# Kernel tuning notes

Hardware: AMD Instinct MI355X
Metric: run time of the kernel (lower is better)

## Reference

```python
import jax, jax.numpy as jnp
import numpy as np

N = 100000   # nodes
E = 1600000  # edges (avg degree 16)
F = 64       # in_feats
H = 128      # hidden_size
O = 10       # out_feats
L = 3        # SAGEConv layers
EPS = 1e-5


def setup_inputs() -> dict:
    key = jax.random.key(0)
    ks = jax.random.split(key, 16)
    s = 0.05
    return {
        "nodes": jax.random.normal(ks[0], (N, F), jnp.float32),
        "src": jax.random.randint(ks[1], (E,), 0, N),
        "dst": jax.random.randint(ks[2], (E,), 0, N),
        # input MLP: Linear(F,H) -> ReLU -> Linear(H,H)
        "W_in1": jax.random.normal(ks[3], (F, H), jnp.float32) * s,
        "b_in1": jnp.zeros((H,), jnp.float32),
        "W_in2": jax.random.normal(ks[4], (H, H), jnp.float32) * s,
        "b_in2": jnp.zeros((H,), jnp.float32),
        # L stacked SAGEConv layers (mean aggregator)
        "W_self": jax.random.normal(ks[5], (L, H, H), jnp.float32) * s,
        "W_neigh": jax.random.normal(ks[6], (L, H, H), jnp.float32) * s,
        "b_sage": jnp.zeros((L, H), jnp.float32),
        "ln_g": jnp.ones((L, H), jnp.float32),
        "ln_b": jnp.zeros((L, H), jnp.float32),
        # output head Linear(H, O)
        "W_out": jax.random.normal(ks[7], (H, O), jnp.float32) * s,
        "b_out": jnp.zeros((O,), jnp.float32),
    }


def reference(nodes, src, dst, W_in1, b_in1, W_in2, b_in2,
              W_self, W_neigh, b_sage, ln_g, ln_b, W_out, b_out):
    # input MLP
    h = jax.nn.relu(nodes @ W_in1 + b_in1) @ W_in2 + b_in2  # [N, H]

    # in-degree for mean aggregation (0-degree nodes get 0 neighbor feature)
    deg = jax.ops.segment_sum(jnp.ones((E,), h.dtype), dst, num_segments=N)
    inv_deg = (1.0 / jnp.maximum(deg, 1.0))[:, None]  # [N, 1]

    for l in range(L):
        # mean over incoming neighbors: gather src feats, scatter-add to dst
        agg = jax.ops.segment_sum(h[src], dst, num_segments=N) * inv_deg  # [N, H]
        h = h @ W_self[l] + agg @ W_neigh[l] + b_sage[l]
        h = jax.nn.relu(h)
        # LayerNorm over feature dim
        mu = h.mean(-1, keepdims=True)
        var = h.var(-1, keepdims=True)
        h = ln_g[l] * (h - mu) * jax.lax.rsqrt(var + EPS) + ln_b[l]

    # dgl.mean_nodes over the single graph -> [1, H]
    g = h.mean(0, keepdims=True)
    return g @ W_out + b_out  # [1, O]
```

## Files before the change

kernel.cpp:

```cpp
#include <hip/hip_runtime.h>
#include <hip/hip_bf16.h>

#define NN 100000
#define NE 1600000
#define FF 64
#define HH 128
#define OO 10
#define NL 3
#define NB 391
#define NBLK 1000
#define CHUNK 1600
#define BCAP 5376
#define LNEPS 1e-5f

typedef short s8v __attribute__((ext_vector_type(8)));
typedef float f32x4 __attribute__((ext_vector_type(4)));
typedef float f32x2 __attribute__((ext_vector_type(2)));

__device__ __forceinline__ unsigned short f2b(float f){
  unsigned u = __float_as_uint(f);
  unsigned r = (u + 0x7FFFu + ((u>>16)&1u)) >> 16;
  return (unsigned short)r;
}

#if __has_builtin(__builtin_amdgcn_cvt_pk_f32_fp8) && __has_builtin(__builtin_amdgcn_cvt_pk_fp8_f32)
__device__ __forceinline__ unsigned char f8enc(float x){
  int p = __builtin_amdgcn_cvt_pk_fp8_f32(x, x, 0, false);
  return (unsigned char)(p & 0xFF);
}
__device__ __forceinline__ void f8dec4(unsigned u, float* o){
  f32x2 lo = __builtin_amdgcn_cvt_pk_f32_fp8(u, false);
  f32x2 hi = __builtin_amdgcn_cvt_pk_f32_fp8(u, true);
  o[0]=lo[0]; o[1]=lo[1]; o[2]=hi[0]; o[3]=hi[1];
}
#else
#include <hip/hip_fp8.h>
__device__ __forceinline__ unsigned char f8enc(float x){
  __hip_fp8_e4m3 q(x); return (unsigned char)q.__x;
}
__device__ __forceinline__ void f8dec4(unsigned u, float* o){
  for(int i=0;i<4;i++){
    __hip_fp8_e4m3 q; q.__x = (unsigned char)(u>>(8*i));
    o[i] = (float)q;
  }
}
#endif

__global__ __launch_bounds__(256) void k_bcount(const int* __restrict__ dst, int* __restrict__ bcnt,
                                                int* __restrict__ blockcnt){
  __shared__ int h[NB];
  for(int i=threadIdx.x;i<NB;i+=256) h[i]=0;
  __syncthreads();
  int base = blockIdx.x*CHUNK;
  for(int i=threadIdx.x;i<CHUNK;i+=256){
    int e = base+i;
    if(e<NE) atomicAdd(&h[((unsigned)dst[e])>>8],1);
  }
  __syncthreads();
  for(int i=threadIdx.x;i<NB;i+=256){
    int v=h[i];
    blockcnt[i*1024 + blockIdx.x] = v;
    if(v) atomicAdd(&bcnt[i],v);
  }
}

__global__ void k_bscan(const int* __restrict__ bcnt, int* __restrict__ boff, int* __restrict__ rowoff){
  __shared__ int s[512];
  int t=threadIdx.x;
  int v = (t<NB)? bcnt[t]:0;
  s[t]=v; __syncthreads();
  for(int off=1;off<512;off<<=1){
    int x=(t>=off)?s[t-off]:0;
    __syncthreads();
    s[t]+=x;
    __syncthreads();
  }
  if(t<NB) boff[t]=s[t]-v;
  if(t==0) rowoff[NN]=NE;
}

__global__ __launch_bounds__(1024) void k_prefix(const int* __restrict__ blockcnt, const int* __restrict__ boff,
                                                 int* __restrict__ pref){
  __shared__ int s[1024];
  int k=blockIdx.x, t=threadIdx.x;
  int v = (t<NBLK)? blockcnt[k*1024+t] : 0;
  s[t]=v; __syncthreads();
  for(int off=1;off<1024;off<<=1){
    int x=(t>=off)?s[t-off]:0;
    __syncthreads();
    s[t]+=x;
    __syncthreads();
  }
  if(t<NBLK) pref[k*1024+t] = boff[k] + s[t]-v;
}

__global__ __launch_bounds__(256) void k_bscatter(const int* __restrict__ src, const int* __restrict__ dst,
                                                  const int* __restrict__ pref, unsigned* __restrict__ ebuf){
  __shared__ int cur[NB];
  __shared__ int pb[NB];
  for(int i=threadIdx.x;i<NB;i+=256){ cur[i]=0; pb[i]=pref[i*1024+blockIdx.x]; }
  __syncthreads();
  int base=blockIdx.x*CHUNK;
  for(int i=threadIdx.x;i<CHUNK;i+=256){
    int e=base+i;
    if(e<NE){
      int d=dst[e];
      int k=((unsigned)d)>>8;
      int r=atomicAdd(&cur[k],1);
      ebuf[pb[k]+r] = (unsigned)src[e] | ((unsigned)(d&255)<<20);
    }
  }
}

__global__ __launch_bounds__(256) void k_bsort(const unsigned* __restrict__ ebuf, const int* __restrict__ bcnt,
                                               const int* __restrict__ boff, int* __restrict__ rowoff,
                                               float* __restrict__ invd, int* __restrict__ csr){
  __shared__ unsigned el[BCAP];
  __shared__ int dg[256], sc[256], cu[256];
  int b=blockIdx.x, t=threadIdx.x;
  int c = bcnt[b]; if(c>BCAP) c=BCAP;
  int base = boff[b];
  for(int i=t;i<c;i+=256) el[i]=ebuf[base+i];
  dg[t]=0;
  __syncthreads();
  for(int i=t;i<c;i+=256) atomicAdd(&dg[el[i]>>20],1);
  __syncthreads();
  int v = dg[t];
  sc[t]=v; __syncthreads();
  for(int off=1;off<256;off<<=1){
    int x=(t>=off)?sc[t-off]:0;
    __syncthreads();
    sc[t]+=x;
    __syncthreads();
  }
  int excl = sc[t]-v;
  int node = b*256+t;
  if(node<NN){
    rowoff[node]=base+excl;
    invd[node]=1.0f/fmaxf((float)v,1.0f);
  }
  cu[t]=excl;
  __syncthreads();
  for(int i=t;i<c;i+=256){
    unsigned e=el[i];
    int d=e>>20;
    int p=atomicAdd(&cu[d],1);
    csr[base+p] = (int)(e & 0xFFFFFu);
  }
}

__global__ void k_repack(const float* __restrict__ W1, const float* __restrict__ W2,
                         const float* __restrict__ Ws, const float* __restrict__ Wn,
                         unsigned short* __restrict__ wf){
  int t = blockIdx.x*256+threadIdx.x;
  if(t >= 122880) return;
  const float* src; int rem;
  if(t < 8192){ src = W1; rem = t; }
  else {
    int u = t - 8192;
    int m = u >> 14; rem = u & 16383;
    if(m==0) src = W2;
    else if(m<=3) src = Ws + (size_t)(m-1)*HH*HH;
    else src = Wn + (size_t)(m-4)*HH*HH;
  }
  int j = rem&7, l=(rem>>3)&63, nt=(rem>>9)&7, kcb=rem>>12;
  int k = kcb*32 + 8*(l>>4) + j;
  int n = nt*16 + (l&15);
  wf[t] = f2b(src[(size_t)k*HH + n]);
}

__global__ __launch_bounds__(256) void k_agg(const uint2* __restrict__ hf8, const int* __restrict__ csr,
                                             const int* __restrict__ rowoff, const float* __restrict__ invd,
                                             uint4* __restrict__ aggb){
  int wave=threadIdx.x>>6, lane=threadIdx.x&63;
  int n = blockIdx.x*4+wave;
  if(n>=NN) return;
  int beg=rowoff[n], end=rowoff[n+1];
  int c = lane&15, q=lane>>4;
  float a0=0.f,a1=0.f,a2=0.f,a3=0.f,a4=0.f,a5=0.f,a6=0.f,a7=0.f;

  int j0 = beg + q;
  int j1 = j0 + 4;
  bool h0 = j0 < end, h1 = j1 < end;
  uint2 u0, u1;
  if(h0) u0 = hf8[(size_t)csr[j0]*16 + c];
  if(h1) u1 = hf8[(size_t)csr[j1]*16 + c];
  while(h0){
    int j2 = j1 + 4;
    bool h2 = j2 < end;
    uint2 u2;
    if(h2) u2 = hf8[(size_t)csr[j2]*16 + c];
    {
      float d0[4], d1[4];
      f8dec4(u0.x,d0); f8dec4(u0.y,d1);
      a0+=d0[0]; a1+=d0[1]; a2+=d0[2]; a3+=d0[3];
      a4+=d1[0]; a5+=d1[1]; a6+=d1[2]; a7+=d1[3];
    }
    u0=u1; h0=h1; j1=j2; u1=u2; h1=h2;
  }

  a0+=__shfl_xor(a0,16); a1+=__shfl_xor(a1,16); a2+=__shfl_xor(a2,16); a3+=__shfl_xor(a3,16);
  a4+=__shfl_xor(a4,16); a5+=__shfl_xor(a5,16); a6+=__shfl_xor(a6,16); a7+=__shfl_xor(a7,16);
  a0+=__shfl_xor(a0,32); a1+=__shfl_xor(a1,32); a2+=__shfl_xor(a2,32); a3+=__shfl_xor(a3,32);
  a4+=__shfl_xor(a4,32); a5+=__shfl_xor(a5,32); a6+=__shfl_xor(a6,32); a7+=__shfl_xor(a7,32);
  if(q==0){
    float s=invd[n];
    uint4 p;
    p.x = (unsigned)f2b(a0*s) | ((unsigned)f2b(a1*s)<<16);
    p.y = (unsigned)f2b(a2*s) | ((unsigned)f2b(a3*s)<<16);
    p.z = (unsigned)f2b(a4*s) | ((unsigned)f2b(a5*s)<<16);
    p.w = (unsigned)f2b(a6*s) | ((unsigned)f2b(a7*s)<<16);
    aggb[(size_t)n*16 + c] = p;
  }
}

__global__ __launch_bounds__(256) void k_mlp(
    const float* __restrict__ X,
    const unsigned short* __restrict__ W1f, const unsigned short* __restrict__ W2f,
    const float* __restrict__ b1, const float* __restrict__ b2,
    unsigned short* __restrict__ hb, unsigned char* __restrict__ hf8)
{
  __shared__ unsigned short tl[64][136];
  int tid=threadIdx.x, l=tid&63, wv=tid>>6, grp=l>>4, lc=l&15;
  int node0 = blockIdx.x*64;
  const s8v* __restrict__ Wv1 = (const s8v*)W1f;
  const s8v* __restrict__ Wv2 = (const s8v*)W2f;
  int r0 = node0 + wv*16 + lc; if(r0>NN-1) r0=NN-1;
  f32x4 acc[8] = {};
  #pragma unroll
  for(int kcb=0;kcb<2;kcb++){
    int k0 = kcb*32 + 8*grp;
    s8v a0;
    float4 fa = *(const float4*)&X[(size_t)r0*FF + k0];
    float4 fb = *(const float4*)&X[(size_t)r0*FF + k0 + 4];
    a0[0]=(short)f2b(fa.x); a0[1]=(short)f2b(fa.y); a0[2]=(short)f2b(fa.z); a0[3]=(short)f2b(fa.w);
    a0[4]=(short)f2b(fb.x); a0[5]=(short)f2b(fb.y); a0[6]=(short)f2b(fb.z); a0[7]=(short)f2b(fb.w);
    #pragma unroll
    for(int nt=0;nt<8;nt++){
      s8v b = Wv1[(kcb*8+nt)*64 + l];
      acc[nt] = __builtin_amdgcn_mfma_f32_16x16x32_bf16(a0, b, acc[nt], 0,0,0);
    }
  }
  #pragma unroll
  for(int r=0;r<4;r++){
    int rr = wv*16 + grp*4 + r;
    #pragma unroll
    for(int nt=0;nt<8;nt++){
      float v = acc[nt][r] + b1[nt*16+lc];
      tl[rr][nt*16+lc] = f2b(fmaxf(v,0.f));
    }
  }
  __syncthreads();
  f32x4 acc2[8] = {};
  #pragma unroll
  for(int kcb=0;kcb<4;kcb++){
    int k0 = kcb*32 + 8*grp;
    s8v a0 = *(const s8v*)&tl[wv*16+lc][k0];
    #pragma unroll
    for(int nt=0;nt<8;nt++){
      s8v b = Wv2[(kcb*8+nt)*64 + l];
      acc2[nt] = __builtin_amdgcn_mfma_f32_16x16x32_bf16(a0, b, acc2[nt], 0,0,0);
    }
  }
  #pragma unroll
  for(int r=0;r<4;r++){
    int node = node0 + wv*16 + grp*4 + r;
    if(node<NN){
      #pragma unroll
      for(int nt=0;nt<8;nt++){
        float v = acc2[nt][r] + b2[nt*16+lc];
        hb[(size_t)node*HH + nt*16 + lc] = f2b(v);
        hf8[(size_t)node*HH + nt*16 + lc] = f8enc(v);
      }
    }
  }
}

template<int K, int DUAL, int RELU, int LN, int F8, int MEAN>
__global__ __launch_bounds__(256) void k_mfma(
    const unsigned short* __restrict__ A, const unsigned short* __restrict__ A2,
    const unsigned short* __restrict__ Wf, const unsigned short* __restrict__ Wf2,
    const float* __restrict__ bias, const float* __restrict__ lng, const float* __restrict__ lnb,
    unsigned short* __restrict__ out, unsigned char* __restrict__ hf8, float* __restrict__ gsum)
{
  constexpr int KC = K/32;
  __shared__ float sm[MEAN ? 4*128 : 4];
  int tid = threadIdx.x;
  int l = tid&63, wv = tid>>6;
  int grp = l>>4, lc = l&15;
  int node0 = blockIdx.x*128;
  const s8v* __restrict__ Wv  = (const s8v*)Wf;
  const s8v* __restrict__ Wv2 = (const s8v*)Wf2;
  f32x4 acc[2][8] = {};
  int r0 = node0 + wv*16 + lc;      if(r0>NN-1) r0=NN-1;
  int r1 = node0 + 64 + wv*16 + lc; if(r1>NN-1) r1=NN-1;
  #pragma unroll
  for(int kcb=0;kcb<KC;kcb++){
    int k0 = kcb*32 + 8*grp;
    s8v a0 = *(const s8v*)&A[(size_t)r0*K + k0];
    s8v a1 = *(const s8v*)&A[(size_t)r1*K + k0];
    s8v c0, c1;
    if(DUAL){
      c0 = *(const s8v*)&A2[(size_t)r0*K + k0];
      c1 = *(const s8v*)&A2[(size_t)r1*K + k0];
    }
    #pragma unroll
    for(int nt=0;nt<8;nt++){
      s8v b = Wv[(kcb*8+nt)*64 + l];
      acc[0][nt] = __builtin_amdgcn_mfma_f32_16x16x32_bf16(a0, b, acc[0][nt], 0,0,0);
      acc[1][nt] = __builtin_amdgcn_mfma_f32_16x16x32_bf16(a1, b, acc[1][nt], 0,0,0);
      if(DUAL){
        s8v b2 = Wv2[(kcb*8+nt)*64 + l];
        acc[0][nt] = __builtin_amdgcn_mfma_f32_16x16x32_bf16(c0, b2, acc[0][nt], 0,0,0);
        acc[1][nt] = __builtin_amdgcn_mfma_f32_16x16x32_bf16(c1, b2, acc[1][nt], 0,0,0);
      }
    }
  }
  float bc[8], gc[8], oc[8];
  #pragma unroll
  for(int nt=0;nt<8;nt++){
    bc[nt] = bias[nt*16+lc];
    if(LN){ gc[nt]=lng[nt*16+lc]; oc[nt]=lnb[nt*16+lc]; }
  }
  float msum[8];
  #pragma unroll
  for(int nt=0;nt<8;nt++) msum[nt]=0.f;
  #pragma unroll
  for(int s2=0;s2<2;s2++){
    #pragma unroll
    for(int r=0;r<4;r++){
      float x[8]; float s=0.f, ss=0.f;
      #pragma unroll
      for(int nt=0;nt<8;nt++){
        float v = acc[s2][nt][r] + bc[nt];
        if(RELU) v = fmaxf(v, 0.f);
        x[nt]=v; s+=v; ss+=v*v;
      }
      if(LN){
        #pragma unroll
        for(int m=1;m<=8;m<<=1){ s+=__shfl_xor(s,m); ss+=__shfl_xor(ss,m); }
        float mu = s*(1.0f/HH);
        float var = ss*(1.0f/HH) - mu*mu;
        float rs = rsqrtf(var + LNEPS);
        #pragma unroll
        for(int nt=0;nt<8;nt++) x[nt] = gc[nt]*(x[nt]-mu)*rs + oc[nt];
      }
      int node = node0 + s2*64 + wv*16 + grp*4 + r;
      if(node<NN){
        if(MEAN){
          #pragma unroll
          for(int nt=0;nt<8;nt++) msum[nt]+=x[nt];
        } else {
          #pragma unroll
          for(int nt=0;nt<8;nt++) out[(size_t)node*HH + nt*16 + lc] = f2b(x[nt]);
          if(F8){
            #pragma unroll
            for(int nt=0;nt<8;nt++) hf8[(size_t)node*HH + nt*16 + lc] = f8enc(x[nt]);
          }
        }
      }
    }
  }
  if(MEAN){
    #pragma unroll
    for(int nt=0;nt<8;nt++){
      msum[nt]+=__shfl_xor(msum[nt],16);
      msum[nt]+=__shfl_xor(msum[nt],32);
    }
    if(grp==0){
      #pragma unroll
      for(int nt=0;nt<8;nt++) sm[wv*128 + nt*16 + lc] = msum[nt];
    }
    __syncthreads();
    if(tid<128){
      float v = sm[tid] + sm[128+tid] + sm[256+tid] + sm[384+tid];
      atomicAdd(&gsum[tid], v);
    }
  }
}

__global__ void k_out(const float* __restrict__ g, const float* __restrict__ Wout,
                      const float* __restrict__ bout, float* __restrict__ out){
  int o=threadIdx.x;
  if(o<OO){
    float acc=bout[o];
    for(int k=0;k<HH;k++) acc = fmaf(g[k]*(1.0f/NN), Wout[k*OO+o], acc);
    out[o]=acc;
  }
}

extern "C" void kernel_launch(void* const* d_in, const int* in_sizes, int n_in,
                              void* d_out, int out_size, void* d_ws, size_t ws_size,
                              hipStream_t stream){
  const float* nodes = (const float*)d_in[0];
  const int*   src   = (const int*)d_in[1];
  const int*   dst   = (const int*)d_in[2];
  const float* W_in1 = (const float*)d_in[3];
  const float* b_in1 = (const float*)d_in[4];
  const float* W_in2 = (const float*)d_in[5];
  const float* b_in2 = (const float*)d_in[6];
  const float* W_self  = (const float*)d_in[7];
  const float* W_neigh = (const float*)d_in[8];
  const float* b_sage  = (const float*)d_in[9];
  const float* ln_g    = (const float*)d_in[10];
  const float* ln_b    = (const float*)d_in[11];
  const float* W_out   = (const float*)d_in[12];
  const float* b_out   = (const float*)d_in[13];

  char* w=(char*)d_ws;
  unsigned short* hb   = (unsigned short*)w; w += (size_t)NN*HH*2;
  unsigned short* aggb = (unsigned short*)w; w += (size_t)NN*HH*2;
  unsigned char*  hf8  = (unsigned char*)w;  w += (size_t)NN*HH;
  unsigned short* wf   = (unsigned short*)w; w += (size_t)122880*2;
  unsigned* ebuf = (unsigned*)w; w += (size_t)NE*4;
  int* csr    = (int*)w;   w += (size_t)NE*4;
  int* rowoff = (int*)w;   w += (size_t)(NN+8)*4;
  float* invd = (float*)w; w += (size_t)NN*4;
  int* bcnt   = (int*)w;   w += (size_t)(NB+1)*4;
  int* boff   = (int*)w;   w += (size_t)(NB+1)*4;
  int* blockcnt=(int*)w;   w += (size_t)NB*1024*4;
  int* pref   = (int*)w;   w += (size_t)NB*1024*4;
  float* gsum = (float*)w; w += 128*4;

  hipMemsetAsync(bcnt, 0, (size_t)(NB+1)*4, stream);
  hipMemsetAsync(gsum, 0, 128*4, stream);

  k_bcount<<<NBLK,256,0,stream>>>(dst,bcnt,blockcnt);
  k_bscan<<<1,512,0,stream>>>(bcnt,boff,rowoff);
  k_prefix<<<NB,1024,0,stream>>>(blockcnt,boff,pref);
  k_bscatter<<<NBLK,256,0,stream>>>(src,dst,pref,ebuf);
  k_bsort<<<NB,256,0,stream>>>(ebuf,bcnt,boff,rowoff,invd,csr);

  k_repack<<<(122880+255)/256,256,0,stream>>>(W_in1,W_in2,W_self,W_neigh,wf);

  const int GB1 = (NN+63)/64;
  const int GB2 = (NN+127)/128;
  k_mlp<<<GB1,256,0,stream>>>(nodes, wf, wf+8192, b_in1, b_in2, hb, hf8);

  for(int l=0;l<NL;l++){
    k_agg<<<(NN+3)/4,256,0,stream>>>((const uint2*)hf8,csr,rowoff,invd,(uint4*)aggb);
    if(l<NL-1)
      k_mfma<HH,1,1,1,1,0><<<GB2,256,0,stream>>>(hb, aggb,
          wf+24576+(size_t)l*16384, wf+73728+(size_t)l*16384,
          b_sage+(size_t)l*HH, ln_g+(size_t)l*HH, ln_b+(size_t)l*HH, hb, hf8, nullptr);
    else
      k_mfma<HH,1,1,1,0,1><<<GB2,256,0,stream>>>(hb, aggb,
          wf+24576+(size_t)l*16384, wf+73728+(size_t)l*16384,
          b_sage+(size_t)l*HH, ln_g+(size_t)l*HH, ln_b+(size_t)l*HH, hb, nullptr, gsum);
  }
  k_out<<<1,64,0,stream>>>(gsum,W_out,b_out,(float*)d_out);
}
```

Before: 393.4 us.

## Fuse neighbor aggregation into SAGE MFMA layer kernel with ping-pong buffers

Merges the separate gather/mean aggregation kernel into the per-layer MFMA kernel. Each block aggregates its 64 nodes' neighbor features into shared memory and then runs the dual GEMM, ReLU and LayerNorm, so the bf16 aggregate no longer makes a round trip through global memory and one launch per layer goes away. Because other blocks still read the previous layer's features, the features are double-buffered across layers. The trade-off is that aggregation now uses 16 lanes per node with a serial walk over edges instead of four edges in parallel, and each block covers 64 nodes instead of 128, so per-node gather latency and weight reloads grow. The fp8 builtin guard was also edited and now checks the same decode builtin twice.

```diff
diff --git a/kernel.cpp b/kernel.cpp
--- a/kernel.cpp
+++ b/kernel.cpp
@@ -23,7 +23,7 @@
   return (unsigned short)r;
 }
 
-#if __has_builtin(__builtin_amdgcn_cvt_pk_f32_fp8) && __has_builtin(__builtin_amdgcn_cvt_pk_fp8_f32)
+#if __has_builtin(__builtin_amdgcn_cvt_pk_f32_fp8) && __has_builtin(__builtin_amdgcn_cvt_pk_f32_fp8)
 __device__ __forceinline__ unsigned char f8enc(float x){
   int p = __builtin_amdgcn_cvt_pk_fp8_f32(x, x, 0, false);
   return (unsigned char)(p & 0xFF);
@@ -169,51 +169,6 @@
   wf[t] = f2b(src[(size_t)k*HH + n]);
 }
 
-__global__ __launch_bounds__(256) void k_agg(const uint2* __restrict__ hf8, const int* __restrict__ csr,
-                                             const int* __restrict__ rowoff, const float* __restrict__ invd,
-                                             uint4* __restrict__ aggb){
-  int wave=threadIdx.x>>6, lane=threadIdx.x&63;
-  int n = blockIdx.x*4+wave;
-  if(n>=NN) return;
-  int beg=rowoff[n], end=rowoff[n+1];
-  int c = lane&15, q=lane>>4;
-  float a0=0.f,a1=0.f,a2=0.f,a3=0.f,a4=0.f,a5=0.f,a6=0.f,a7=0.f;
-
-  int j0 = beg + q;
-  int j1 = j0 + 4;
-  bool h0 = j0 < end, h1 = j1 < end;
-  uint2 u0, u1;
-  if(h0) u0 = hf8[(size_t)csr[j0]*16 + c];
-  if(h1) u1 = hf8[(size_t)csr[j1]*16 + c];
-  while(h0){
-    int j2 = j1 + 4;
-    bool h2 = j2 < end;
-    uint2 u2;
-    if(h2) u2 = hf8[(size_t)csr[j2]*16 + c];
-    {
-      float d0[4], d1[4];
-      f8dec4(u0.x,d0); f8dec4(u0.y,d1);
-      a0+=d0[0]; a1+=d0[1]; a2+=d0[2]; a3+=d0[3];
-      a4+=d1[0]; a5+=d1[1]; a6+=d1[2]; a7+=d1[3];
-    }
-    u0=u1; h0=h1; j1=j2; u1=u2; h1=h2;
-  }
-
-  a0+=__shfl_xor(a0,16); a1+=__shfl_xor(a1,16); a2+=__shfl_xor(a2,16); a3+=__shfl_xor(a3,16);
-  a4+=__shfl_xor(a4,16); a5+=__shfl_xor(a5,16); a6+=__shfl_xor(a6,16); a7+=__shfl_xor(a7,16);
-  a0+=__shfl_xor(a0,32); a1+=__shfl_xor(a1,32); a2+=__shfl_xor(a2,32); a3+=__shfl_xor(a3,32);
-  a4+=__shfl_xor(a4,32); a5+=__shfl_xor(a5,32); a6+=__shfl_xor(a6,32); a7+=__shfl_xor(a7,32);
-  if(q==0){
-    float s=invd[n];
-    uint4 p;
-    p.x = (unsigned)f2b(a0*s) | ((unsigned)f2b(a1*s)<<16);
-    p.y = (unsigned)f2b(a2*s) | ((unsigned)f2b(a3*s)<<16);
-    p.z = (unsigned)f2b(a4*s) | ((unsigned)f2b(a5*s)<<16);
-    p.w = (unsigned)f2b(a6*s) | ((unsigned)f2b(a7*s)<<16);
-    aggb[(size_t)n*16 + c] = p;
-  }
-}
-
 __global__ __launch_bounds__(256) void k_mlp(
     const float* __restrict__ X,
     const unsigned short* __restrict__ W1f, const unsigned short* __restrict__ W2f,
@@ -276,92 +231,111 @@
   }
 }
 
-template<int K, int DUAL, int RELU, int LN, int F8, int MEAN>
-__global__ __launch_bounds__(256) void k_mfma(
-    const unsigned short* __restrict__ A, const unsigned short* __restrict__ A2,
-    const unsigned short* __restrict__ Wf, const unsigned short* __restrict__ Wf2,
+template<int LAST>
+__global__ __launch_bounds__(256) void k_fused(
+    const unsigned short* __restrict__ hb_in, const unsigned char* __restrict__ hf8_in,
+    const int* __restrict__ csr, const int* __restrict__ rowoff, const float* __restrict__ invd,
+    const unsigned short* __restrict__ Wsf, const unsigned short* __restrict__ Wnf,
     const float* __restrict__ bias, const float* __restrict__ lng, const float* __restrict__ lnb,
-    unsigned short* __restrict__ out, unsigned char* __restrict__ hf8, float* __restrict__ gsum)
+    unsigned short* __restrict__ hb_out, unsigned char* __restrict__ hf8_out, float* __restrict__ gsum)
 {
-  constexpr int KC = K/32;
-  __shared__ float sm[MEAN ? 4*128 : 4];
-  int tid = threadIdx.x;
-  int l = tid&63, wv = tid>>6;
-  int grp = l>>4, lc = l&15;
-  int node0 = blockIdx.x*128;
-  const s8v* __restrict__ Wv  = (const s8v*)Wf;
-  const s8v* __restrict__ Wv2 = (const s8v*)Wf2;
-  f32x4 acc[2][8] = {};
-  int r0 = node0 + wv*16 + lc;      if(r0>NN-1) r0=NN-1;
-  int r1 = node0 + 64 + wv*16 + lc; if(r1>NN-1) r1=NN-1;
-  #pragma unroll
-  for(int kcb=0;kcb<KC;kcb++){
+  __shared__ unsigned short agg[64][136];
+  __shared__ float sm[LAST ? 4*128 : 4];
+  int tid=threadIdx.x, l=tid&63, wv=tid>>6, grp=l>>4, lc=l&15;
+  int node0 = blockIdx.x*64;
+  {
+    int q = tid>>4, c = tid&15;
+    const uint2* __restrict__ hv = (const uint2*)hf8_in;
+    #pragma unroll
+    for(int rnd=0;rnd<4;rnd++){
+      int ln = q + rnd*16;
+      int n = node0 + ln;
+      float a0=0.f,a1=0.f,a2=0.f,a3=0.f,a4=0.f,a5=0.f,a6=0.f,a7=0.f;
+      if(n<NN){
+        int beg=rowoff[n], end=rowoff[n+1];
+        int j0=beg, j1=beg+1;
+        bool h0=j0<end, h1=j1<end;
+        uint2 u0,u1;
+        if(h0) u0 = hv[(size_t)csr[j0]*16 + c];
+        if(h1) u1 = hv[(size_t)csr[j1]*16 + c];
+        while(h0){
+          int j2=j1+1; bool h2=j2<end; uint2 u2;
+          if(h2) u2 = hv[(size_t)csr[j2]*16 + c];
+          float d0[4], d1[4];
+          f8dec4(u0.x,d0); f8dec4(u0.y,d1);
+          a0+=d0[0]; a1+=d0[1]; a2+=d0[2]; a3+=d0[3];
+          a4+=d1[0]; a5+=d1[1]; a6+=d1[2]; a7+=d1[3];
+          u0=u1; h0=h1; u1=u2; h1=h2; j1=j2;
+        }
+        float s=invd[n];
+        a0*=s; a1*=s; a2*=s; a3*=s; a4*=s; a5*=s; a6*=s; a7*=s;
+      }
+      uint4 p;
+      p.x = (unsigned)f2b(a0) | ((unsigned)f2b(a1)<<16);
+      p.y = (unsigned)f2b(a2) | ((unsigned)f2b(a3)<<16);
+      p.z = (unsigned)f2b(a4) | ((unsigned)f2b(a5)<<16);
+      p.w = (unsigned)f2b(a6) | ((unsigned)f2b(a7)<<16);
+      *(uint4*)&agg[ln][c*8] = p;
+    }
+  }
+  __syncthreads();
+  const s8v* __restrict__ Wv  = (const s8v*)Wsf;
+  const s8v* __restrict__ Wv2 = (const s8v*)Wnf;
+  int r0 = node0 + wv*16 + lc; if(r0>NN-1) r0=NN-1;
+  int lr = wv*16 + lc;
+  f32x4 acc[8] = {};
+  #pragma unroll
+  for(int kcb=0;kcb<4;kcb++){
     int k0 = kcb*32 + 8*grp;
-    s8v a0 = *(const s8v*)&A[(size_t)r0*K + k0];
-    s8v a1 = *(const s8v*)&A[(size_t)r1*K + k0];
-    s8v c0, c1;
-    if(DUAL){
-      c0 = *(const s8v*)&A2[(size_t)r0*K + k0];
-      c1 = *(const s8v*)&A2[(size_t)r1*K + k0];
-    }
-    #pragma unroll
-    for(int nt=0;nt<8;nt++){
-      s8v b = Wv[(kcb*8+nt)*64 + l];
-      acc[0][nt] = __builtin_amdgcn_mfma_f32_16x16x32_bf16(a0, b, acc[0][nt], 0,0,0);
-      acc[1][nt] = __builtin_amdgcn_mfma_f32_16x16x32_bf16(a1, b, acc[1][nt], 0,0,0);
-      if(DUAL){
-        s8v b2 = Wv2[(kcb*8+nt)*64 + l];
-        acc[0][nt] = __builtin_amdgcn_mfma_f32_16x16x32_bf16(c0, b2, acc[0][nt], 0,0,0);
-        acc[1][nt] = __builtin_amdgcn_mfma_f32_16x16x32_bf16(c1, b2, acc[1][nt], 0,0,0);
-      }
+    s8v a0 = *(const s8v*)&hb_in[(size_t)r0*HH + k0];
+    s8v c0 = *(const s8v*)&agg[lr][k0];
+    #pragma unroll
+    for(int nt=0;nt<8;nt++){
+      s8v b  = Wv[(kcb*8+nt)*64 + l];
+      s8v b2 = Wv2[(kcb*8+nt)*64 + l];
+      acc[nt] = __builtin_amdgcn_mfma_f32_16x16x32_bf16(a0, b,  acc[nt], 0,0,0);
+      acc[nt] = __builtin_amdgcn_mfma_f32_16x16x32_bf16(c0, b2, acc[nt], 0,0,0);
     }
   }
   float bc[8], gc[8], oc[8];
   #pragma unroll
   for(int nt=0;nt<8;nt++){
     bc[nt] = bias[nt*16+lc];
-    if(LN){ gc[nt]=lng[nt*16+lc]; oc[nt]=lnb[nt*16+lc]; }
+    gc[nt]=lng[nt*16+lc]; oc[nt]=lnb[nt*16+lc];
   }
   float msum[8];
   #pragma unroll
   for(int nt=0;nt<8;nt++) msum[nt]=0.f;
   #pragma unroll
-  for(int s2=0;s2<2;s2++){
-    #pragma unroll
-    for(int r=0;r<4;r++){
-      float x[8]; float s=0.f, ss=0.f;
-      #pragma unroll
-      for(int nt=0;nt<8;nt++){
-        float v = acc[s2][nt][r] + bc[nt];
-        if(RELU) v = fmaxf(v, 0.f);
-        x[nt]=v; s+=v; ss+=v*v;
+  for(int r=0;r<4;r++){
+    float x[8]; float s=0.f, ss=0.f;
+    #pragma unroll
+    for(int nt=0;nt<8;nt++){
+      float v = acc[nt][r] + bc[nt];
+      v = fmaxf(v, 0.f);
+      x[nt]=v; s+=v; ss+=v*v;
+    }
+    #pragma unroll
+    for(int m=1;m<=8;m<<=1){ s+=__shfl_xor(s,m); ss+=__shfl_xor(ss,m); }
+    float mu = s*(1.0f/HH);
+    float var = ss*(1.0f/HH) - mu*mu;
+    float rs = rsqrtf(var + LNEPS);
+    #pragma unroll
+    for(int nt=0;nt<8;nt++) x[nt] = gc[nt]*(x[nt]-mu)*rs + oc[nt];
+    int node = node0 + wv*16 + grp*4 + r;
+    if(node<NN){
+      if(LAST){
+        #pragma unroll
+        for(int nt=0;nt<8;nt++) msum[nt]+=x[nt];
+      } else {
+        #pragma unroll
+        for(int nt=0;nt<8;nt++) hb_out[(size_t)node*HH + nt*16 + lc] = f2b(x[nt]);
+        #pragma unroll
+        for(int nt=0;nt<8;nt++) hf8_out[(size_t)node*HH + nt*16 + lc] = f8enc(x[nt]);
       }
-      if(LN){
-        #pragma unroll
-        for(int m=1;m<=8;m<<=1){ s+=__shfl_xor(s,m); ss+=__shfl_xor(ss,m); }
-        float mu = s*(1.0f/HH);
-        float var = ss*(1.0f/HH) - mu*mu;
-        float rs = rsqrtf(var + LNEPS);
-        #pragma unroll
-        for(int nt=0;nt<8;nt++) x[nt] = gc[nt]*(x[nt]-mu)*rs + oc[nt];
-      }
-      int node = node0 + s2*64 + wv*16 + grp*4 + r;
-      if(node<NN){
-        if(MEAN){
-          #pragma unroll
-          for(int nt=0;nt<8;nt++) msum[nt]+=x[nt];
-        } else {
-          #pragma unroll
-          for(int nt=0;nt<8;nt++) out[(size_t)node*HH + nt*16 + lc] = f2b(x[nt]);
-          if(F8){
-            #pragma unroll
-            for(int nt=0;nt<8;nt++) hf8[(size_t)node*HH + nt*16 + lc] = f8enc(x[nt]);
-          }
-        }
-      }
-    }
-  }
-  if(MEAN){
+    }
+  }
+  if(LAST){
     #pragma unroll
     for(int nt=0;nt<8;nt++){
       msum[nt]+=__shfl_xor(msum[nt],16);
@@ -408,9 +382,10 @@
   const float* b_out   = (const float*)d_in[13];
 
   char* w=(char*)d_ws;
-  unsigned short* hb   = (unsigned short*)w; w += (size_t)NN*HH*2;
-  unsigned short* aggb = (unsigned short*)w; w += (size_t)NN*HH*2;
-  unsigned char*  hf8  = (unsigned char*)w;  w += (size_t)NN*HH;
+  unsigned short* hb0  = (unsigned short*)w; w += (size_t)NN*HH*2;
+  unsigned short* hb1  = (unsigned short*)w; w += (size_t)NN*HH*2;
+  unsigned char*  hf80 = (unsigned char*)w;  w += (size_t)NN*HH;
+  unsigned char*  hf81 = (unsigned char*)w;  w += (size_t)NN*HH;
   unsigned short* wf   = (unsigned short*)w; w += (size_t)122880*2;
   unsigned* ebuf = (unsigned*)w; w += (size_t)NE*4;
   int* csr    = (int*)w;   w += (size_t)NE*4;
@@ -434,19 +409,23 @@
   k_repack<<<(122880+255)/256,256,0,stream>>>(W_in1,W_in2,W_self,W_neigh,wf);
 
   const int GB1 = (NN+63)/64;
-  const int GB2 = (NN+127)/128;
-  k_mlp<<<GB1,256,0,stream>>>(nodes, wf, wf+8192, b_in1, b_in2, hb, hf8);
-
+  k_mlp<<<GB1,256,0,stream>>>(nodes, wf, wf+8192, b_in1, b_in2, hb0, hf80);
+
+  unsigned short* hbs[2] = {hb0, hb1};
+  unsigned char*  hfs[2] = {hf80, hf81};
   for(int l=0;l<NL;l++){
-    k_agg<<<(NN+3)/4,256,0,stream>>>((const uint2*)hf8,csr,rowoff,invd,(uint4*)aggb);
+    const unsigned short* Wsf = wf+24576+(size_t)l*16384;
+    const unsigned short* Wnf = wf+73728+(size_t)l*16384;
+    unsigned short* hin  = hbs[l&1];
+    unsigned char*  fin  = hfs[l&1];
+    unsigned short* hout = hbs[(l+1)&1];
+    unsigned char*  fout = hfs[(l+1)&1];
     if(l<NL-1)
-      k_mfma<HH,1,1,1,1,0><<<GB2,256,0,stream>>>(hb, aggb,
-          wf+24576+(size_t)l*16384, wf+73728+(size_t)l*16384,
-          b_sage+(size_t)l*HH, ln_g+(size_t)l*HH, ln_b+(size_t)l*HH, hb, hf8, nullptr);
+      k_fused<0><<<GB1,256,0,stream>>>(hin, fin, csr, rowoff, invd, Wsf, Wnf,
+          b_sage+(size_t)l*HH, ln_g+(size_t)l*HH, ln_b+(size_t)l*HH, hout, fout, nullptr);
     else
-      k_mfma<HH,1,1,1,0,1><<<GB2,256,0,stream>>>(hb, aggb,
-          wf+24576+(size_t)l*16384, wf+73728+(size_t)l*16384,
-          b_sage+(size_t)l*HH, ln_g+(size_t)l*HH, ln_b+(size_t)l*HH, hb, nullptr, gsum);
+      k_fused<1><<<GB1,256,0,stream>>>(hin, fin, csr, rowoff, invd, Wsf, Wnf,
+          b_sage+(size_t)l*HH, ln_g+(size_t)l*HH, ln_b+(size_t)l*HH, nullptr, nullptr, gsum);
   }
   k_out<<<1,64,0,stream>>>(gsum,W_out,b_out,(float*)d_out);
 }
```

After: 539.1 us. 37.0% more time.
